# Kernel tuning notes

Measured on AMD Instinct MI355X. Metric: run time of the kernel, lower is better.

The kernel has to match this reference:

```python
import jax, jax.numpy as jnp
import numpy as np

V, D, B, L = 10000, 300, 64, 128
CF = 5.0   # concentrator_factor
EPS = 1e-8  # torch cosine_similarity eps


def setup_inputs() -> dict:
    key = jax.random.key(0)
    ks = jax.random.split(key, 7)
    concepts_list = jax.random.randint(ks[0], (B, L), 0, V)
    concepts_length = jax.random.randint(ks[1], (B,), 0, L + 1)
    embed_w = jax.random.normal(ks[2], (V, D), jnp.float32)
    concept_w = jax.random.normal(ks[3], (V, D), jnp.float32)
    em = jax.random.uniform(ks[4], (V, V), jnp.float32)
    # init_params normalization: row-max minus col-min, per row
    rng = (em.max(axis=1) - em.min(axis=0))[:, None]
    edge_matrix = em / (rng + (rng == 0).astype(em.dtype))
    affectiveness = jax.random.uniform(ks[5], (V,), jnp.float32)
    lam = jax.random.uniform(ks[6], (V,), jnp.float32)
    return {
        "concepts_list": concepts_list,
        "concepts_length": concepts_length,
        "embed_w": embed_w,
        "concept_w": concept_w,
        "edge_matrix": edge_matrix,
        "affectiveness": affectiveness,
        "lam": lam,
    }


def reference(concepts_list, concepts_length, embed_w, concept_w, edge_matrix, affectiveness, lam):
    b, l = concepts_list.shape
    mask = (jnp.arange(l)[None, :] < concepts_length[:, None]).astype(embed_w.dtype)  # [B,L]
    denom = jnp.maximum(concepts_length, 1).astype(embed_w.dtype)[:, None]            # [B,1]

    # context representation: ragged per-sample mean, then mean over batch
    ce = embed_w[concepts_list]                                  # [B,L,D]
    per_sample = (ce * mask[:, :, None]).sum(axis=1) / denom     # [B,D] (zeros for empty)
    context = per_sample.mean(axis=0)                            # [D]

    # |cosine similarity| of context vs every concept embedding row
    cn = jnp.linalg.norm(context)
    rn = jnp.linalg.norm(concept_w, axis=1)                      # [V]
    cos = jnp.abs((concept_w @ context) / jnp.maximum(cn * rn, EPS))  # [V]

    em = edge_matrix[concepts_list]                              # [B,L,V]
    rel = em * cos
    aff = (em > 0).astype(em.dtype) * affectiveness
    weights = lam * rel + (1.0 - lam) * aff                      # [B,L,V]
    probs = jax.nn.softmax(weights * CF, axis=2)                 # [B,L,V]
    ce2 = jnp.einsum('blv,vd->bld', probs, concept_w)            # [B,L,D]

    out = (ce2 * mask[:, :, None]).sum(axis=1) / denom           # [B,D] (zeros for empty)
    return out
```

## Files before the change

kernel.cpp:

```cpp
#include <hip/hip_runtime.h>
#include <math.h>

#define NV 10000
#define ND 300
#define NB 64
#define NL 128
#define CFv 5.0f
#define EPSV 1e-8f

#define WS_CTX   0
#define WS_CN    300
#define WS_CNT   301
#define WS_A     320
#define WS_B     10320
#define WS_ROWS  20320
#define WS_S     28512
#define WS_CUM   36704
#define WS_WTG   36800

#define KR    128
#define WTGLD 10112
#define NKR   79
#define GMB   8
#define NTI   19
#define MT    32
#define MTOT  1024

typedef __attribute__((ext_vector_type(8))) __bf16 bf16x8;
typedef __attribute__((ext_vector_type(4))) float f32x4;

static __device__ __forceinline__ unsigned short f2bf(float x) {
  union { float f; unsigned u; } v; v.f = x;
  unsigned r = v.u + 0x7fffu + ((v.u >> 16) & 1u);
  return (unsigned short)(r >> 16);
}

__global__ __launch_bounds__(256) void k_init(float* __restrict__ out, float* __restrict__ wsf) {
  int g = blockIdx.x * 256 + threadIdx.x;
  if (g < NB * ND) out[g] = 0.f;
  if (g < 302) wsf[g] = 0.f;
}

#define CSL 4
__global__ __launch_bounds__(320) void k_context(const int* __restrict__ clist,
                                                 const int* __restrict__ clen,
                                                 const float* __restrict__ embed,
                                                 float* __restrict__ wsf) {
  __shared__ int kl[NL];
  int b = blockIdx.x / CSL, sl = blockIdx.x % CSL;
  int d = threadIdx.x;
  int len = clen[b];
  if (d < NL) kl[d] = clist[b * NL + d];
  __syncthreads();
  if (d >= ND) return;
  float acc = 0.f;
  for (int l = sl; l < len; l += CSL)
    acc += embed[(long)kl[l] * ND + d];
  float dn = (float)(len > 0 ? len : 1);
  atomicAdd(&wsf[WS_CTX + d], acc * (1.0f / NB) / dn);
}

__global__ __launch_bounds__(320) void k_cn(float* __restrict__ wsf) {
  __shared__ float red[5];
  int t = threadIdx.x;
  float x = (t < ND) ? wsf[WS_CTX + t] : 0.f;
  float s = x * x;
  #pragma unroll
  for (int o = 32; o; o >>= 1) s += __shfl_xor(s, o);
  if ((t & 63) == 0) red[t >> 6] = s;
  __syncthreads();
  if (t == 0) {
    float tot = 0.f;
    #pragma unroll
    for (int i = 0; i < 5; ++i) tot += red[i];
    wsf[WS_CN] = sqrtf(tot);
  }
}

__global__ __launch_bounds__(256) void k_cos(const float* __restrict__ cw,
                                             const float* __restrict__ lam,
                                             const float* __restrict__ aff,
                                             float* __restrict__ wsf) {
  int wid = threadIdx.x >> 6, lane = threadIdx.x & 63;
  int v = blockIdx.x * 4 + wid;
  const float* row = cw + (long)v * ND;
  float dot = 0.f, rn2 = 0.f;
  for (int d = lane; d < ND; d += 64) {
    float w = row[d], c = wsf[WS_CTX + d];
    dot += w * c;
    rn2 += w * w;
  }
  #pragma unroll
  for (int o = 32; o; o >>= 1) { dot += __shfl_xor(dot, o); rn2 += __shfl_xor(rn2, o); }
  if (lane == 0) {
    float cn = wsf[WS_CN];
    float cosv = fabsf(dot) / fmaxf(cn * sqrtf(rn2), EPSV);
    float lv = lam[v];
    wsf[WS_A + v] = CFv * lv * cosv;
    wsf[WS_B + v] = CFv * (1.f - lv) * aff[v];
  }
}

__global__ __launch_bounds__(256) void k_wt(const float* __restrict__ cw, float* __restrict__ wsf) {
  __shared__ unsigned short T[304][68];
  int tid = threadIdx.x;
  int v0 = blockIdx.x * 64;
  for (int q = tid; q < 304 * 68 / 2; q += 256) ((unsigned*)&T[0][0])[q] = 0u;
  __syncthreads();
  const float4* cw4 = (const float4*)cw;
  for (int q = tid; q < 64 * 75; q += 256) {
    int r = q / 75, p = q - r * 75;
    int v = v0 + r;
    if (v < NV) {
      float4 w = cw4[(long)v * 75 + p];
      T[4 * p + 0][r] = f2bf(w.x);
      T[4 * p + 1][r] = f2bf(w.y);
      T[4 * p + 2][r] = f2bf(w.z);
      T[4 * p + 3][r] = f2bf(w.w);
    }
  }
  __syncthreads();
  unsigned short* wtg = (unsigned short*)(wsf + WS_WTG);
  for (int q = tid; q < 304 * 16; q += 256) {
    int n = q >> 4, rp = q & 15;
    *(ushort4*)&wtg[(long)n * WTGLD + v0 + 4 * rp] = *(const ushort4*)&T[n][4 * rp];
  }
}

__global__ __launch_bounds__(256) void k_compact(const int* __restrict__ clen, int* __restrict__ wsi) {
  __shared__ int cum[NB + 1];
  int tid = threadIdx.x;
  if (tid < 64) {
    int ln = clen[tid]; ln = min(max(ln, 0), NL);
    int s = ln;
    #pragma unroll
    for (int o = 1; o < 64; o <<= 1) {
      int t = __shfl_up(s, o);
      if (tid >= o) s += t;
    }
    cum[tid + 1] = s;
    if (tid == 0) cum[0] = 0;
    if (tid == 63) wsi[WS_CNT] = s;
  }
  __syncthreads();
  if (tid <= NB) wsi[WS_CUM + tid] = cum[tid];
  int t = blockIdx.x * 256 + tid;
  int b = t >> 7, l = t & 127;
  int len = cum[b + 1] - cum[b];
  if (l < len) wsi[WS_ROWS + cum[b] + l] = t;
}

__global__ __launch_bounds__(256) void k_srow(const int* __restrict__ clist,
                                              const float* __restrict__ edge,
                                              float* __restrict__ wsf) {
  const int* wsi = (const int*)wsf;
  int wid = threadIdx.x >> 6, lane = threadIdx.x & 63;
  int pos = blockIdx.x * 4 + wid;
  int count = wsi[WS_CNT];
  if (pos >= count) return;
  int row = wsi[WS_ROWS + pos];
  const float4* e4 = (const float4*)(edge + (long)clist[row] * NV);
  const float4* A4 = (const float4*)(wsf + WS_A);
  const float4* B4 = (const float4*)(wsf + WS_B);
  float sp = 0.f;
  for (int v = lane; v < NV / 4; v += 64) {
    float4 em = e4[v], a = A4[v], b = B4[v];
    sp += __expf(fmaf(a.x, em.x, (em.x > 0.f) ? b.x : 0.f));
    sp += __expf(fmaf(a.y, em.y, (em.y > 0.f) ? b.y : 0.f));
    sp += __expf(fmaf(a.z, em.z, (em.z > 0.f) ? b.z : 0.f));
    sp += __expf(fmaf(a.w, em.w, (em.w > 0.f) ? b.w : 0.f));
  }
  #pragma unroll
  for (int o = 32; o; o >>= 1) sp += __shfl_xor(sp, o);
  if (lane == 0) wsf[WS_S + pos] = sp;
}

__global__ __launch_bounds__(512, 4) void k_main(const int* __restrict__ clist,
                                                 const int* __restrict__ clen,
                                                 const float* __restrict__ edge,
                                                 const float* __restrict__ wsf,
                                                 float* __restrict__ out) {
  __shared__ __align__(16) float raw[2][MT * KR];
  __shared__ __align__(16) unsigned short ebuf[2][MT * KR];
  __shared__ float cls[2][KR];
  __shared__ float sout[GMB][304];
  __shared__ int   rofs[MTOT];
  __shared__ int   bv[MTOT];
  __shared__ float sclv[MTOT];

  const int* wsi = (const int*)wsf;
  const unsigned short* wtg = (const unsigned short*)(wsf + WS_WTG);
  int tid = threadIdx.x;
  int kr = blockIdx.x >> 3, g = blockIdx.x & 7;
  int v0 = kr * KR;
  int klen = NV - v0; if (klen > KR) klen = KR;
  int nch = (klen + 31) >> 5;
  int bs = g * GMB;
  int r0 = wsi[WS_CUM + bs], r1 = wsi[WS_CUM + bs + GMB];
  int nrows = r1 - r0;
  int ntiles = (nrows + MT - 1) >> 5;

  int wv = tid >> 6, lane = tid & 63;
  int q4 = lane >> 4, l15 = lane & 15;
  int nt0 = (wv * NTI) >> 3, nt1 = ((wv + 1) * NTI) >> 3;

  bf16x8 bfrag[3][4] = {};
  #pragma unroll
  for (int j = 0; j < 3; ++j)
    #pragma unroll
    for (int c5 = 0; c5 < 4; ++c5)
      if (nt0 + j < nt1 && c5 < nch) {
        int n = (nt0 + j) * 16 + l15;
        bfrag[j][c5] = *(const bf16x8*)(const void*)&wtg[(long)n * WTGLD + v0 + c5 * 32 + q4 * 8];
      }

  for (int q = tid; q < 2 * KR; q += 512) {
    int a = q >> 7, k = q & (KR - 1);
    float val = 0.f;
    if (v0 + k < NV) val = wsf[(a ? WS_B : WS_A) + v0 + k];
    cls[a][k] = val;
  }
  for (int q = tid; q < GMB * 304; q += 512) ((float*)sout)[q] = 0.f;
  for (int i = tid; i < MTOT; i += 512) {
    int ro = 0, b = -1; float sc = 0.f;
    if (i < nrows) {
      int rowid = wsi[WS_ROWS + r0 + i];
      ro = clist[rowid] * NV;
      b = rowid >> 7;
      float S = wsf[WS_S + r0 + i];
      int ln = clen[b];
      sc = 1.0f / (S * (float)(ln > 0 ? ln : 1));
    }
    rofs[i] = ro; bv[i] = b; sclv[i] = sc;
  }
  __syncthreads();

  int rm0 = tid >> 5;
  int kq0 = (tid & 31) * 4;
  int vkq = v0 + ((kq0 < klen) ? kq0 : 0);

  auto issue_dma = [&](int buf, int tt) {
    int i0 = tt * MT + rm0;
    const float* s0 = edge + (long)rofs[i0] + vkq;
    const float* s1 = edge + (long)rofs[i0 + 16] + vkq;
    __builtin_amdgcn_global_load_lds(
        (const __attribute__((address_space(1))) unsigned int*)s0,
        (__attribute__((address_space(3))) unsigned int*)&raw[buf][tid * 4], 16, 0, 0);
    __builtin_amdgcn_global_load_lds(
        (const __attribute__((address_space(1))) unsigned int*)s1,
        (__attribute__((address_space(3))) unsigned int*)&raw[buf][2048 + tid * 4], 16, 0, 0);
  };

  int curb = -1;
  float rs0 = 0.f, rs1 = 0.f, rs2 = 0.f;
  auto emit = [&](int b, float s0, float s1, float s2) {
    if (b < 0) return;
    int rel = b - bs;
    #pragma unroll
    for (int j = 0; j < 3; ++j) {
      if (nt0 + j < nt1) {
        int n = (nt0 + j) * 16 + l15;
        if (n < ND) {
          float v = (j == 0) ? s0 : (j == 1) ? s1 : s2;
          atomicAdd(&sout[rel][n], v);
        }
      }
    }
  };

  if (ntiles > 0) {
    issue_dma(0, 0);

    for (int t = 0; t < ntiles; ++t) {
      int cur = t & 1;
      if (t + 1 < ntiles) {
        issue_dma(cur ^ 1, t + 1);
        asm volatile("s_waitcnt vmcnt(2)" ::: "memory");
      } else {
        asm volatile("s_waitcnt vmcnt(0)" ::: "memory");
      }
      __builtin_amdgcn_sched_barrier(0);

      {
        float4 em0 = *(const float4*)&raw[cur][tid * 4];
        float4 em1 = *(const float4*)&raw[cur][2048 + tid * 4];
        float4 a = *(const float4*)&cls[0][kq0];
        float4 b = *(const float4*)&cls[1][kq0];
        ushort4 e0, e1;
        e0.x = f2bf(__expf(fmaf(a.x, em0.x, (em0.x > 0.f) ? b.x : 0.f)));
        e0.y = f2bf(__expf(fmaf(a.y, em0.y, (em0.y > 0.f) ? b.y : 0.f)));
        e0.z = f2bf(__expf(fmaf(a.z, em0.z, (em0.z > 0.f) ? b.z : 0.f)));
        e0.w = f2bf(__expf(fmaf(a.w, em0.w, (em0.w > 0.f) ? b.w : 0.f)));
        e1.x = f2bf(__expf(fmaf(a.x, em1.x, (em1.x > 0.f) ? b.x : 0.f)));
        e1.y = f2bf(__expf(fmaf(a.y, em1.y, (em1.y > 0.f) ? b.y : 0.f)));
        e1.z = f2bf(__expf(fmaf(a.z, em1.z, (em1.z > 0.f) ? b.z : 0.f)));
        e1.w = f2bf(__expf(fmaf(a.w, em1.w, (em1.w > 0.f) ? b.w : 0.f)));
        int bo = (tid & 31) << 3;
        int off0 = ((rm0 << 8) + bo) ^ ((rm0 & 7) << 4);
        int off1 = (((rm0 + 16) << 8) + bo) ^ ((rm0 & 7) << 4);
        *(ushort4*)((char*)&ebuf[cur][0] + off0) = e0;
        *(ushort4*)((char*)&ebuf[cur][0] + off1) = e1;
      }

      asm volatile("s_waitcnt lgkmcnt(0)" ::: "memory");
      __builtin_amdgcn_s_barrier();
      __builtin_amdgcn_sched_barrier(0);

      f32x4 acc[2][3] = {};
      const char* eb = (const char*)&ebuf[cur][0];
      #pragma unroll
      for (int c5 = 0; c5 < 4; ++c5) {
        if (c5 < nch) {
          int kb2 = (c5 * 32 + q4 * 8) << 1;
          int off0 = ((l15 << 8) + kb2) ^ ((l15 & 7) << 4);
          int off1 = (((16 + l15) << 8) + kb2) ^ ((l15 & 7) << 4);
          bf16x8 a0 = *(const bf16x8*)(const void*)(eb + off0);
          bf16x8 a1 = *(const bf16x8*)(const void*)(eb + off1);
          #pragma unroll
          for (int j = 0; j < 3; ++j) {
            if (nt0 + j < nt1) {
              acc[0][j] = __builtin_amdgcn_mfma_f32_16x16x32_bf16(a0, bfrag[j][c5], acc[0][j], 0, 0, 0);
              acc[1][j] = __builtin_amdgcn_mfma_f32_16x16x32_bf16(a1, bfrag[j][c5], acc[1][j], 0, 0, 0);
            }
          }
        }
      }
      #pragma unroll
      for (int ms = 0; ms < 2; ++ms)
        #pragma unroll
        for (int r = 0; r < 4; ++r) {
          int m = ms * 16 + q4 * 4 + r;
          int i = t * MT + m;
          int b = bv[i];
          if (b >= 0) {
            float sc = sclv[i];
            if (b != curb) {
              emit(curb, rs0, rs1, rs2);
              curb = b; rs0 = rs1 = rs2 = 0.f;
            }
            rs0 += acc[ms][0][r] * sc;
            rs1 += acc[ms][1][r] * sc;
            rs2 += acc[ms][2][r] * sc;
          }
        }
    }
    emit(curb, rs0, rs1, rs2);
  }
  __syncthreads();

  for (int q = tid; q < GMB * 304; q += 512) {
    int s = q / 304, n = q - s * 304;
    float v = sout[s][n];
    if (n < ND && v != 0.f) atomicAdd(&out[(bs + s) * ND + n], v);
  }
}

extern "C" void kernel_launch(void* const* d_in, const int* in_sizes, int n_in,
                              void* d_out, int out_size, void* d_ws, size_t ws_size,
                              hipStream_t stream) {
  const int*   clist = (const int*)d_in[0];
  const int*   clen  = (const int*)d_in[1];
  const float* embed = (const float*)d_in[2];
  const float* cw    = (const float*)d_in[3];
  const float* edge  = (const float*)d_in[4];
  const float* aff   = (const float*)d_in[5];
  const float* lam   = (const float*)d_in[6];
  float* out = (float*)d_out;
  float* wsf = (float*)d_ws;
  int*   wsi = (int*)d_ws;

  hipLaunchKernelGGL(k_init,    dim3(77),          dim3(256), 0, stream, out, wsf);
  hipLaunchKernelGGL(k_context, dim3(NB * CSL),    dim3(320), 0, stream, clist, clen, embed, wsf);
  hipLaunchKernelGGL(k_cn,      dim3(1),           dim3(320), 0, stream, wsf);
  hipLaunchKernelGGL(k_cos,     dim3(NV / 4),      dim3(256), 0, stream, cw, lam, aff, wsf);
  hipLaunchKernelGGL(k_wt,      dim3(WTGLD / 64),  dim3(256), 0, stream, cw, wsf);
  hipLaunchKernelGGL(k_compact, dim3(32),          dim3(256), 0, stream, clen, wsi);
  hipLaunchKernelGGL(k_srow,    dim3(NB * NL / 4), dim3(256), 0, stream, clist, edge, wsf);
  hipLaunchKernelGGL(k_main,    dim3(NKR * 8),     dim3(512), 0, stream,
                     clist, clen, edge, wsf, out);
}
```

Before: 211.7 us.

## Halve k_main vocab tile and prefetch edge rows into registers

The vocab tile per block drops from 128 to 64 columns, doubling the grid to 157x8 blocks of 256 threads, each wave owning about five N-tiles instead of three. The async global-to-LDS DMA into a raw float buffer is replaced by a register prefetch of the next tile's edge values, issued before the MFMA loop, with exp/bf16 conversion written into the alternate LDS buffer after it. This removes the raw LDS staging buffer and aims to overlap global loads with MFMA work while raising the number of blocks. The cost is more blocks re-reading per-batch setup (rows, offsets, scales), more LDS atomics to the output scratch, and higher register use from the larger accumulator arrays.

```diff
diff --git a/kernel.cpp b/kernel.cpp
--- a/kernel.cpp
+++ b/kernel.cpp
@@ -18,9 +18,9 @@
 #define WS_CUM   36704
 #define WS_WTG   36800
 
-#define KR    128
+#define KR    64
 #define WTGLD 10112
-#define NKR   79
+#define NKR   157
 #define GMB   8
 #define NTI   19
 #define MT    32
@@ -175,12 +175,11 @@
   if (lane == 0) wsf[WS_S + pos] = sp;
 }
 
-__global__ __launch_bounds__(512, 4) void k_main(const int* __restrict__ clist,
+__global__ __launch_bounds__(256, 4) void k_main(const int* __restrict__ clist,
                                                  const int* __restrict__ clen,
                                                  const float* __restrict__ edge,
                                                  const float* __restrict__ wsf,
                                                  float* __restrict__ out) {
-  __shared__ __align__(16) float raw[2][MT * KR];
   __shared__ __align__(16) unsigned short ebuf[2][MT * KR];
   __shared__ float cls[2][KR];
   __shared__ float sout[GMB][304];
@@ -202,26 +201,26 @@
 
   int wv = tid >> 6, lane = tid & 63;
   int q4 = lane >> 4, l15 = lane & 15;
-  int nt0 = (wv * NTI) >> 3, nt1 = ((wv + 1) * NTI) >> 3;
-
-  bf16x8 bfrag[3][4] = {};
+  int nt0 = (wv * NTI) >> 2, nt1 = ((wv + 1) * NTI) >> 2;
+
+  bf16x8 bfrag[5][2] = {};
   #pragma unroll
-  for (int j = 0; j < 3; ++j)
-    #pragma unroll
-    for (int c5 = 0; c5 < 4; ++c5)
+  for (int j = 0; j < 5; ++j)
+    #pragma unroll
+    for (int c5 = 0; c5 < 2; ++c5)
       if (nt0 + j < nt1 && c5 < nch) {
         int n = (nt0 + j) * 16 + l15;
         bfrag[j][c5] = *(const bf16x8*)(const void*)&wtg[(long)n * WTGLD + v0 + c5 * 32 + q4 * 8];
       }
 
-  for (int q = tid; q < 2 * KR; q += 512) {
-    int a = q >> 7, k = q & (KR - 1);
+  for (int q = tid; q < 2 * KR; q += 256) {
+    int a = q >> 6, k = q & (KR - 1);
     float val = 0.f;
     if (v0 + k < NV) val = wsf[(a ? WS_B : WS_A) + v0 + k];
     cls[a][k] = val;
   }
-  for (int q = tid; q < GMB * 304; q += 512) ((float*)sout)[q] = 0.f;
-  for (int i = tid; i < MTOT; i += 512) {
+  for (int q = tid; q < GMB * 304; q += 256) ((float*)sout)[q] = 0.f;
+  for (int i = tid; i < MTOT; i += 256) {
     int ro = 0, b = -1; float sc = 0.f;
     if (i < nrows) {
       int rowid = wsi[WS_ROWS + r0 + i];
@@ -235,89 +234,81 @@
   }
   __syncthreads();
 
-  int rm0 = tid >> 5;
-  int kq0 = (tid & 31) * 4;
-  int vkq = v0 + ((kq0 < klen) ? kq0 : 0);
-
-  auto issue_dma = [&](int buf, int tt) {
-    int i0 = tt * MT + rm0;
-    const float* s0 = edge + (long)rofs[i0] + vkq;
-    const float* s1 = edge + (long)rofs[i0 + 16] + vkq;
-    __builtin_amdgcn_global_load_lds(
-        (const __attribute__((address_space(1))) unsigned int*)s0,
-        (__attribute__((address_space(3))) unsigned int*)&raw[buf][tid * 4], 16, 0, 0);
-    __builtin_amdgcn_global_load_lds(
-        (const __attribute__((address_space(1))) unsigned int*)s1,
-        (__attribute__((address_space(3))) unsigned int*)&raw[buf][2048 + tid * 4], 16, 0, 0);
+  int rm_s = tid >> 4;
+  int k4 = tid & 15;
+  int kvalid = (k4 * 4 < klen);
+  int vkq = v0 + (kvalid ? k4 * 4 : 0);
+
+  float4 eld[2];
+  int    vld[2];
+
+  auto stage_load = [&](int tt, bool valid) {
+    #pragma unroll
+    for (int j = 0; j < 2; ++j) {
+      vld[j] = 0;
+      int i0 = tt * MT + rm_s + 16 * j;
+      if (valid && kvalid && i0 < nrows) {
+        eld[j] = *(const float4*)(edge + (long)rofs[i0] + vkq);
+        vld[j] = 1;
+      }
+    }
   };
 
+  auto stage_write = [&](int nb) {
+    char* eb = (char*)&ebuf[nb][0];
+    #pragma unroll
+    for (int j = 0; j < 2; ++j) {
+      ushort4 ev = make_ushort4(0, 0, 0, 0);
+      if (vld[j]) {
+        float4 a = *(const float4*)&cls[0][k4 * 4];
+        float4 b = *(const float4*)&cls[1][k4 * 4];
+        float4 em = eld[j];
+        ev.x = f2bf(__expf(fmaf(a.x, em.x, (em.x > 0.f) ? b.x : 0.f)));
+        ev.y = f2bf(__expf(fmaf(a.y, em.y, (em.y > 0.f) ? b.y : 0.f)));
+        ev.z = f2bf(__expf(fmaf(a.z, em.z, (em.z > 0.f) ? b.z : 0.f)));
+        ev.w = f2bf(__expf(fmaf(a.w, em.w, (em.w > 0.f) ? b.w : 0.f)));
+      }
+      int row = rm_s + 16 * j;
+      int off = ((row << 7) + (k4 << 3)) ^ ((row & 7) << 4);
+      *(ushort4*)(eb + off) = ev;
+    }
+  };
+
   int curb = -1;
-  float rs0 = 0.f, rs1 = 0.f, rs2 = 0.f;
-  auto emit = [&](int b, float s0, float s1, float s2) {
+  float rs[5] = {0.f, 0.f, 0.f, 0.f, 0.f};
+  auto emit = [&](int b) {
     if (b < 0) return;
     int rel = b - bs;
     #pragma unroll
-    for (int j = 0; j < 3; ++j) {
+    for (int j = 0; j < 5; ++j) {
       if (nt0 + j < nt1) {
         int n = (nt0 + j) * 16 + l15;
-        if (n < ND) {
-          float v = (j == 0) ? s0 : (j == 1) ? s1 : s2;
-          atomicAdd(&sout[rel][n], v);
-        }
+        if (n < ND) atomicAdd(&sout[rel][n], rs[j]);
       }
     }
   };
 
   if (ntiles > 0) {
-    issue_dma(0, 0);
+    stage_load(0, true);
+    stage_write(0);
+    __syncthreads();
 
     for (int t = 0; t < ntiles; ++t) {
       int cur = t & 1;
-      if (t + 1 < ntiles) {
-        issue_dma(cur ^ 1, t + 1);
-        asm volatile("s_waitcnt vmcnt(2)" ::: "memory");
-      } else {
-        asm volatile("s_waitcnt vmcnt(0)" ::: "memory");
-      }
-      __builtin_amdgcn_sched_barrier(0);
-
-      {
-        float4 em0 = *(const float4*)&raw[cur][tid * 4];
-        float4 em1 = *(const float4*)&raw[cur][2048 + tid * 4];
-        float4 a = *(const float4*)&cls[0][kq0];
-        float4 b = *(const float4*)&cls[1][kq0];
-        ushort4 e0, e1;
-        e0.x = f2bf(__expf(fmaf(a.x, em0.x, (em0.x > 0.f) ? b.x : 0.f)));
-        e0.y = f2bf(__expf(fmaf(a.y, em0.y, (em0.y > 0.f) ? b.y : 0.f)));
-        e0.z = f2bf(__expf(fmaf(a.z, em0.z, (em0.z > 0.f) ? b.z : 0.f)));
-        e0.w = f2bf(__expf(fmaf(a.w, em0.w, (em0.w > 0.f) ? b.w : 0.f)));
-        e1.x = f2bf(__expf(fmaf(a.x, em1.x, (em1.x > 0.f) ? b.x : 0.f)));
-        e1.y = f2bf(__expf(fmaf(a.y, em1.y, (em1.y > 0.f) ? b.y : 0.f)));
-        e1.z = f2bf(__expf(fmaf(a.z, em1.z, (em1.z > 0.f) ? b.z : 0.f)));
-        e1.w = f2bf(__expf(fmaf(a.w, em1.w, (em1.w > 0.f) ? b.w : 0.f)));
-        int bo = (tid & 31) << 3;
-        int off0 = ((rm0 << 8) + bo) ^ ((rm0 & 7) << 4);
-        int off1 = (((rm0 + 16) << 8) + bo) ^ ((rm0 & 7) << 4);
-        *(ushort4*)((char*)&ebuf[cur][0] + off0) = e0;
-        *(ushort4*)((char*)&ebuf[cur][0] + off1) = e1;
-      }
-
-      asm volatile("s_waitcnt lgkmcnt(0)" ::: "memory");
-      __builtin_amdgcn_s_barrier();
-      __builtin_amdgcn_sched_barrier(0);
-
-      f32x4 acc[2][3] = {};
+      stage_load(t + 1, t + 1 < ntiles);
+
+      f32x4 acc[2][5] = {};
       const char* eb = (const char*)&ebuf[cur][0];
       #pragma unroll
-      for (int c5 = 0; c5 < 4; ++c5) {
+      for (int c5 = 0; c5 < 2; ++c5) {
         if (c5 < nch) {
-          int kb2 = (c5 * 32 + q4 * 8) << 1;
-          int off0 = ((l15 << 8) + kb2) ^ ((l15 & 7) << 4);
-          int off1 = (((16 + l15) << 8) + kb2) ^ ((l15 & 7) << 4);
+          int kb2 = (c5 << 6) + (q4 << 4);
+          int off0 = ((l15 << 7) + kb2) ^ ((l15 & 7) << 4);
+          int off1 = (((16 + l15) << 7) + kb2) ^ ((l15 & 7) << 4);
           bf16x8 a0 = *(const bf16x8*)(const void*)(eb + off0);
           bf16x8 a1 = *(const bf16x8*)(const void*)(eb + off1);
           #pragma unroll
-          for (int j = 0; j < 3; ++j) {
+          for (int j = 0; j < 5; ++j) {
             if (nt0 + j < nt1) {
               acc[0][j] = __builtin_amdgcn_mfma_f32_16x16x32_bf16(a0, bfrag[j][c5], acc[0][j], 0, 0, 0);
               acc[1][j] = __builtin_amdgcn_mfma_f32_16x16x32_bf16(a1, bfrag[j][c5], acc[1][j], 0, 0, 0);
@@ -325,6 +316,9 @@
           }
         }
       }
+
+      stage_write(cur ^ 1);
+
       #pragma unroll
       for (int ms = 0; ms < 2; ++ms)
         #pragma unroll
@@ -335,20 +329,23 @@
           if (b >= 0) {
             float sc = sclv[i];
             if (b != curb) {
-              emit(curb, rs0, rs1, rs2);
-              curb = b; rs0 = rs1 = rs2 = 0.f;
+              emit(curb);
+              curb = b;
+              #pragma unroll
+              for (int j = 0; j < 5; ++j) rs[j] = 0.f;
             }
-            rs0 += acc[ms][0][r] * sc;
-            rs1 += acc[ms][1][r] * sc;
-            rs2 += acc[ms][2][r] * sc;
+            #pragma unroll
+            for (int j = 0; j < 5; ++j) rs[j] += acc[ms][j][r] * sc;
           }
         }
-    }
-    emit(curb, rs0, rs1, rs2);
-  }
-  __syncthreads();
-
-  for (int q = tid; q < GMB * 304; q += 512) {
+
+      __syncthreads();
+    }
+    emit(curb);
+  }
+  __syncthreads();
+
+  for (int q = tid; q < GMB * 304; q += 256) {
     int s = q / 304, n = q - s * 304;
     float v = sout[s][n];
     if (n < ND && v != 0.f) atomicAdd(&out[(bs + s) * ND + n], v);
@@ -376,6 +373,6 @@
   hipLaunchKernelGGL(k_wt,      dim3(WTGLD / 64),  dim3(256), 0, stream, cw, wsf);
   hipLaunchKernelGGL(k_compact, dim3(32),          dim3(256), 0, stream, clen, wsi);
   hipLaunchKernelGGL(k_srow,    dim3(NB * NL / 4), dim3(256), 0, stream, clist, edge, wsf);
-  hipLaunchKernelGGL(k_main,    dim3(NKR * 8),     dim3(512), 0, stream,
+  hipLaunchKernelGGL(k_main,    dim3(NKR * 8),     dim3(256), 0, stream,
                      clist, clen, edge, wsf, out);
 }
```

After: 230.3 us. 8.8% more time.
